# Kernel tuning notes

Measured on AMD Instinct MI355X. Metric: run time of the kernel, lower is better.

The kernel has to match this reference:

```python
import jax, jax.numpy as jnp
import numpy as np

B, S, D = 2, 2048, 1024
H, DK = 16, 64          # n_heads, d_kv; inner_dim = H*DK = D
NUM_BUCKETS = 32        # T5 relative_attention_num_buckets
MAX_DIST = 128          # T5 relative_attention_max_distance
SM_SCALE = 1.0 / np.sqrt(H)  # module uses 1/sqrt(n_heads), not 1/sqrt(d_kv)


def setup_inputs() -> dict:
    key = jax.random.key(0)
    ks = jax.random.split(key, 6)
    w = 0.02  # typical init scale for projection weights
    return {
        "hidden_states": jax.random.normal(ks[0], (B, S, D), jnp.float32),
        "Wq": jax.random.normal(ks[1], (D, H * DK), jnp.float32) * w,
        "Wk": jax.random.normal(ks[2], (D, H * DK), jnp.float32) * w,
        "Wv": jax.random.normal(ks[3], (D, H * DK), jnp.float32) * w,
        "Wo": jax.random.normal(ks[4], (H * DK, D), jnp.float32) * w,
        "rel_bias": jax.random.normal(ks[5], (NUM_BUCKETS, H), jnp.float32) * w,
    }


def _relative_position_buckets(qlen, klen):
    """T5 bidirectional relative-position bucketing -> [qlen, klen] int32."""
    ctx = jnp.arange(qlen, dtype=jnp.int32)[:, None]
    mem = jnp.arange(klen, dtype=jnp.int32)[None, :]
    rp = mem - ctx  # relative position
    nb = NUM_BUCKETS // 2  # bidirectional split
    ret = (rp > 0).astype(jnp.int32) * nb
    rpa = jnp.abs(rp)
    max_exact = nb // 2
    is_small = rpa < max_exact
    rpf = jnp.maximum(rpa, 1).astype(jnp.float32)
    large = max_exact + (
        jnp.log(rpf / max_exact) / np.log(MAX_DIST / max_exact) * (nb - max_exact)
    ).astype(jnp.int32)
    large = jnp.minimum(large, nb - 1)
    return ret + jnp.where(is_small, rpa, large)


def reference(hidden_states, Wq, Wk, Wv, Wo, rel_bias):
    b, s, d = hidden_states.shape
    q = (hidden_states @ Wq).reshape(b, s, H, DK)
    k = (hidden_states @ Wk).reshape(b, s, H, DK)
    v = (hidden_states @ Wv).reshape(b, s, H, DK)

    buckets = _relative_position_buckets(s, s)        # [S, S]
    bias = rel_bias[buckets]                          # [S, S, H]
    bias = jnp.transpose(bias, (2, 0, 1))[None]       # [1, H, S, S]

    scores = jnp.einsum("bqhd,bkhd->bhqk", q, k) * SM_SCALE + bias
    attn = jax.nn.softmax(scores, axis=-1)
    out = jnp.einsum("bhqk,bkhd->bqhd", attn, v).reshape(b, s, H * DK)
    return out @ Wo
```

## Files before the change

kernel.cpp:

```cpp
#include <hip/hip_runtime.h>
#include <math.h>


typedef _Float16 f16;
typedef _Float16 f16x4 __attribute__((ext_vector_type(4)));
typedef _Float16 f16x8 __attribute__((ext_vector_type(8)));
typedef float f32x4 __attribute__((ext_vector_type(4)));
typedef float f32x16 __attribute__((ext_vector_type(16)));
typedef unsigned int u32;
typedef u32 u32x4 __attribute__((ext_vector_type(4)));

#define MFMA16(a, b, c) __builtin_amdgcn_mfma_f32_16x16x32_f16((a), (b), (c), 0, 0, 0)
#define MFMA32(a, b, c) __builtin_amdgcn_mfma_f32_32x32x16_f16((a), (b), (c), 0, 0, 0)

static __device__ __forceinline__ float EXP2(float x) {
  float r;
  asm("v_exp_f32 %0, %1" : "=v"(r) : "v"(x));
  return r;
}

static __device__ __forceinline__ u32 pk2(float a, float b) {
  return __builtin_bit_cast(u32, __builtin_amdgcn_cvt_pkrtz(a, b));
}
static __device__ __forceinline__ void swap32(u32& a, u32& b) {
  asm volatile("v_permlane32_swap_b32 %0, %1" : "+v"(a), "+v"(b));
}

#define KEEPV8(v8)                                                        \
  do {                                                                    \
    u32x4 _t = __builtin_bit_cast(u32x4, (v8));                           \
    asm volatile("" ::"v"(_t[0]), "v"(_t[1]), "v"(_t[2]), "v"(_t[3]));    \
  } while (0)

__device__ __forceinline__ void gload16(const f16* g, f16* l) {
  __builtin_amdgcn_global_load_lds(
      (const __attribute__((address_space(1))) void*)g,
      (__attribute__((address_space(3))) void*)l, 16, 0, 0);
}


__global__ __launch_bounds__(256) void cast_x_kernel(const float4* __restrict__ x,
                                                     f16x4* __restrict__ xh) {
  int i = blockIdx.x * 256 + threadIdx.x;
  float4 v = x[i];
  f16x4 o;
  o[0] = (f16)v.x; o[1] = (f16)v.y; o[2] = (f16)v.z; o[3] = (f16)v.w;
  xh[i] = o;
}

__global__ void transpose_w_kernel(const float* __restrict__ w0, const float* __restrict__ w1,
                                   const float* __restrict__ w2, const float* __restrict__ w3,
                                   f16* __restrict__ wt) {
  int z = blockIdx.z;
  const float* w = (z == 0) ? w0 : (z == 1) ? w1 : (z == 2) ? w2 : w3;
  float sc = (z == 0) ? 0.36067376022224085f : 1.0f;
  __shared__ float tile[32][33];
  int tx = threadIdx.x, ty = threadIdx.y;
  int kt = blockIdx.x * 32, nt = blockIdx.y * 32;
#pragma unroll
  for (int i = 0; i < 4; ++i)
    tile[ty + i * 8][tx] = w[(size_t)(kt + ty + i * 8) * 1024 + nt + tx];
  __syncthreads();
#pragma unroll
  for (int i = 0; i < 4; ++i)
    wt[((size_t)z * 1024 + nt + ty + i * 8) * 1024 + kt + tx] = (f16)(tile[tx][ty + i * 8] * sc);
}

__global__ void transpose_v_kernel(const f16* __restrict__ vin, f16* __restrict__ vout) {
  __shared__ f16 tile[32][33];
  int bh = blockIdx.z;
  int s0 = blockIdx.x * 32, d0 = blockIdx.y * 32;
  int tx = threadIdx.x, ty = threadIdx.y;
  const f16* src = vin + ((size_t)bh * 2048 + s0) * 64 + d0;
#pragma unroll
  for (int i = 0; i < 4; ++i) tile[ty + i * 8][tx] = src[(size_t)(ty + i * 8) * 64 + tx];
  __syncthreads();
  f16* dst = vout + ((size_t)bh * 64 + d0) * 2048 + s0;
#pragma unroll
  for (int i = 0; i < 4; ++i) dst[(size_t)(ty + i * 8) * 2048 + tx] = tile[tx][ty + i * 8];
}

__global__ __launch_bounds__(256) void bias_kernel(const float* __restrict__ rel_bias,
                                                   f16* __restrict__ bias_rel) {
  int idx = blockIdx.x * 256 + threadIdx.x;
  int h = idx >> 12;
  int r = idx & 4095;
  int rp = r - 2048;
  if (rp < -2047) rp = -2047;
  int bucket = (rp > 0) ? 16 : 0;
  int rpa = (rp < 0) ? -rp : rp;
  if (rpa < 8) {
    bucket += rpa;
  } else {
    int large = 8 + (int)(logf((float)rpa / 8.0f) / logf(16.0f) * 8.0f);
    bucket += (large < 15) ? large : 15;
  }
  bias_rel[idx] = (f16)(rel_bias[bucket * 16 + h] * 1.4426950408889634f);
}

__device__ __forceinline__ void gemm128_core(const f16* __restrict__ A, const f16* __restrict__ Bt,
                                             int mrow, int ncol0, f16* sm ,
                                             f32x4 acc[4][4]) {
  const int t = threadIdx.x;
  const int lane = t & 63, w = t >> 6;
  const int cL = lane & 15, g = lane >> 4;
  const int wr = w >> 1, wc = w & 1;

  const int c0 = w * 128 + lane;
  const int c1 = c0 + 64;
  const int rA0 = c0 >> 2, kA0 = ((c0 & 3) ^ (rA0 & 3)) << 3;
  const int rA1 = c1 >> 2, kA1 = ((c1 & 3) ^ (rA1 & 3)) << 3;
  const f16* gA0 = A + (size_t)(mrow + rA0) * 1024 + kA0;
  const f16* gA1 = A + (size_t)(mrow + rA1) * 1024 + kA1;
  const f16* gB0 = Bt + (size_t)(ncol0 + rA0) * 1024 + kA0;
  const f16* gB1 = Bt + (size_t)(ncol0 + rA1) * 1024 + kA1;
  const int lds0 = (w * 2) * 512, lds1 = (w * 2 + 1) * 512;

#define GSTAGE(buf, k0)                            \
  do {                                             \
    f16* s_ = sm + (buf) * 8192;                   \
    gload16(gA0 + (k0), s_ + lds0);                \
    gload16(gA1 + (k0), s_ + lds1);                \
    gload16(gB0 + (k0), s_ + 4096 + lds0);         \
    gload16(gB1 + (k0), s_ + 4096 + lds1);         \
  } while (0)

  GSTAGE(0, 0);
  __syncthreads();
#pragma unroll 2
  for (int ks = 0; ks < 32; ++ks) {
    const int cur = ks & 1;
    if (ks < 31) GSTAGE(cur ^ 1, (ks + 1) * 32);
    const f16* bA = sm + cur * 8192;
    const f16* bB = bA + 4096;
    f16x8 af[4], bf[4];
#pragma unroll
    for (int m = 0; m < 4; ++m) {
      int r = wr * 64 + m * 16 + cL;
      af[m] = *(const f16x8*)&bA[r * 32 + ((g ^ (r & 3)) << 3)];
    }
#pragma unroll
    for (int n = 0; n < 4; ++n) {
      int r = wc * 64 + n * 16 + cL;
      bf[n] = *(const f16x8*)&bB[r * 32 + ((g ^ (r & 3)) << 3)];
    }
#pragma unroll
    for (int m = 0; m < 4; ++m)
#pragma unroll
      for (int n = 0; n < 4; ++n) acc[m][n] = MFMA16(af[m], bf[n], acc[m][n]);
    __syncthreads();
  }
#undef GSTAGE
}

__global__ __launch_bounds__(256) void gemm_qkv_kernel(const f16* __restrict__ Xh,
                                                       const f16* __restrict__ Wt,
                                                       f16* __restrict__ Qh,
                                                       f16* __restrict__ Kh,
                                                       f16* __restrict__ Vrow) {
  __shared__ __align__(16) f16 sm[2][8192];
  int mrow = blockIdx.y * 128, ncol0 = blockIdx.x * 128;
  f32x4 acc[4][4] = {};
  gemm128_core(Xh, Wt, mrow, ncol0, &sm[0][0], acc);
  int lane = threadIdx.x & 63, w = threadIdx.x >> 6;
  int cL = lane & 15, g = lane >> 4;
  int wr = w >> 1, wc = w & 1;
  int which = (ncol0 + wc * 64) >> 10;
  f16* dst = (which == 0) ? Qh : (which == 1) ? Kh : Vrow;
#pragma unroll
  for (int m = 0; m < 4; ++m) {
#pragma unroll
    for (int n = 0; n < 4; ++n) {
#pragma unroll
      for (int r = 0; r < 4; ++r) {
        int tt = mrow + wr * 64 + m * 16 + g * 4 + r;
        int b = tt >> 11, s = tt & 2047;
        int col = (ncol0 + wc * 64 + n * 16 + cL) & 1023;
        int hh = col >> 6, dk = col & 63;
        dst[(((size_t)b * 16 + hh) * 2048 + s) * 64 + dk] = (f16)acc[m][n][r];
      }
    }
  }
}

__global__ __launch_bounds__(256) void gemm_out_kernel(const f16* __restrict__ Oh,
                                                       const f16* __restrict__ WoT,
                                                       float* __restrict__ out) {
  __shared__ __align__(16) f16 sm[2][8192];
  int mrow = blockIdx.y * 128, ncol0 = blockIdx.x * 128;
  f32x4 acc[4][4] = {};
  gemm128_core(Oh, WoT, mrow, ncol0, &sm[0][0], acc);
  int lane = threadIdx.x & 63, w = threadIdx.x >> 6;
  int cL = lane & 15, g = lane >> 4;
  int wr = w >> 1, wc = w & 1;
#pragma unroll
  for (int m = 0; m < 4; ++m)
#pragma unroll
    for (int n = 0; n < 4; ++n)
#pragma unroll
      for (int r = 0; r < 4; ++r) {
        int tt = mrow + wr * 64 + m * 16 + g * 4 + r;
        out[(size_t)tt * 1024 + ncol0 + wc * 64 + n * 16 + cL] = acc[m][n][r];
      }
}

__global__ __launch_bounds__(512) void attn_kernel(const f16* __restrict__ Qh,
                                                   const f16* __restrict__ Kh,
                                                   const f16* __restrict__ Vt,
                                                   const f16* __restrict__ bias_rel,
                                                   f16* __restrict__ Oh) {
  __shared__ __align__(16) f16 sKV[2][2][8192];
  __shared__ __align__(16) f16 sB[2176];
  const int p = blockIdx.x;
  const int L = ((p & 7) << 6) + (p >> 3);
  const int bh = L >> 4;
  const int qt = (L & 15) << 7;
  const int h = bh & 15, b = bh >> 4;
  int t = threadIdx.x;
  int lane = t & 63, wave = t >> 6;
  const int gr = wave >> 2, sw = wave & 3;
  int lo5 = lane & 31, hi = lane >> 5;
  const size_t bhS = (size_t)bh * 2048;
  const int qrow = qt + sw * 32 + lo5;

  const f16* qp = Qh + (bhS + qrow) * 64 + hi * 8;
  f16x8 qf[4];
#pragma unroll
  for (int m = 0; m < 4; ++m) qf[m] = *(const f16x8*)(qp + 16 * m);

  float cpos = (float)bias_rel[(size_t)h * 4096 + 4095];
  float cneg = (float)bias_rel[(size_t)h * 4096 + 1];

#pragma unroll
  for (int m = 0; m < 4; ++m) KEEPV8(qf[m]);
  asm volatile("" ::"v"(cpos), "v"(cneg));

  {
    const float4* gB = (const float4*)(bias_rel + (size_t)h * 4096 + 1920 - qt);
    for (int i = t; i < 272; i += 512) ((float4*)sB)[i] = gB[i];
  }

  const int tg = t & 255;
  const int rK0 = tg >> 3, ccK0 = ((tg & 7) ^ (rK0 & 7)) << 3;
  const int rK1 = rK0 + 32, ccK1 = ((tg & 7) ^ (rK1 & 7)) << 3;
  const f16* gK0 = Kh + (bhS + rK0) * 64 + ccK0;
  const f16* gK1 = Kh + (bhS + rK1) * 64 + ccK1;
  const f16* gV0 = Vt + ((size_t)bh * 64 + rK0) * 2048 + ccK0;
  const f16* gV1 = Vt + ((size_t)bh * 64 + rK1) * 2048 + ccK1;
  const int ldsA = sw * 512, ldsB = sw * 512 + 2048;

#define ASTAGE(buf, key0)                           \
  do {                                              \
    f16* s_ = &sKV[gr][buf][0];                     \
    gload16(gK0 + (size_t)(key0) * 64, s_ + ldsA);  \
    gload16(gK1 + (size_t)(key0) * 64, s_ + ldsB);  \
    gload16(gV0 + (key0), s_ + 4096 + ldsA);        \
    gload16(gV1 + (key0), s_ + 4096 + ldsB);        \
  } while (0)

  f32x16 o0 = {}, o1 = {};
  float m_ = -INFINITY, lsum = 0.f;
  const int sw7 = lo5 & 7;
  const int kbase = gr << 10;

  ASTAGE(0, kbase);
  asm volatile("s_waitcnt lgkmcnt(0)" ::: "memory");

  for (int it = 0; it < 16; ++it) {
    asm volatile("s_waitcnt vmcnt(0)" ::: "memory");
    __builtin_amdgcn_s_barrier();
    if (it < 15) ASTAGE((it + 1) & 1, kbase + (it + 1) * 64);

    const int key0 = kbase + it * 64;
    const f16* kb = &sKV[gr][it & 1][0];
    const f16* vb = kb + 4096;
    const int dkt = key0 - qt;

    f32x16 sa0, sa1;
    if (dkt >= 256 || dkt <= -192) {
      float c = (dkt > 0) ? cpos : cneg;
#pragma unroll
      for (int i = 0; i < 16; ++i) { sa0[i] = c; sa1[i] = c; }
    } else {
      const int bb = key0 + 4 * hi - sw * 32 - lo5 + 128;
#pragma unroll
      for (int i = 0; i < 16; ++i) {
        int pat = (i & 3) + 8 * (i >> 2);
        sa0[i] = (float)sB[bb + pat];
        sa1[i] = (float)sB[bb + 32 + pat];
      }
    }
    const f16* kr0 = kb + lo5 * 64;
    const f16* kr1 = kb + (32 + lo5) * 64;
    __builtin_amdgcn_s_setprio(1);
#pragma unroll
    for (int m = 0; m < 4; ++m) {
      int c = ((2 * m + hi) ^ sw7) << 3;
      sa0 = MFMA32(*(const f16x8*)(kr0 + c), qf[m], sa0);
      sa1 = MFMA32(*(const f16x8*)(kr1 + c), qf[m], sa1);
    }
    __builtin_amdgcn_s_setprio(0);
    float tm[16];
#pragma unroll
    for (int i = 0; i < 16; ++i) tm[i] = fmaxf(sa0[i], sa1[i]);
#pragma unroll
    for (int s2 = 8; s2; s2 >>= 1)
#pragma unroll
      for (int i = 0; i < 8; ++i)
        if (i < s2) tm[i] = fmaxf(tm[i], tm[i + s2]);
    float mx = fmaxf(tm[0], __shfl_xor(tm[0], 32));
    if (__any(mx > m_ + 8.f)) {
      float mn = fmaxf(m_, mx);
      float corr = EXP2(m_ - mn);
      lsum *= corr;
      m_ = mn;
#pragma unroll
      for (int i = 0; i < 16; ++i) { o0[i] *= corr; o1[i] *= corr; }
    }
    float pr[16];
    u32 w0, w1, w2, w3, w4, w5, w6, w7;
#pragma unroll
    for (int i = 0; i < 16; ++i) pr[i] = EXP2(sa0[i] - m_);
    w0 = pk2(pr[0], pr[1]);   w1 = pk2(pr[2], pr[3]);
    w2 = pk2(pr[4], pr[5]);   w3 = pk2(pr[6], pr[7]);
    w4 = pk2(pr[8], pr[9]);   w5 = pk2(pr[10], pr[11]);
    w6 = pk2(pr[12], pr[13]); w7 = pk2(pr[14], pr[15]);
#pragma unroll
    for (int s2 = 8; s2; s2 >>= 1)
#pragma unroll
      for (int i = 0; i < 8; ++i)
        if (i < s2) pr[i] += pr[i + s2];
    float ls = pr[0];
    swap32(w0, w2); swap32(w1, w3); swap32(w4, w6); swap32(w5, w7);
    f16x8 pb0 = __builtin_bit_cast(f16x8, (u32x4){w0, w1, w2, w3});
    f16x8 pb1 = __builtin_bit_cast(f16x8, (u32x4){w4, w5, w6, w7});
#pragma unroll
    for (int i = 0; i < 16; ++i) pr[i] = EXP2(sa1[i] - m_);
    w0 = pk2(pr[0], pr[1]);   w1 = pk2(pr[2], pr[3]);
    w2 = pk2(pr[4], pr[5]);   w3 = pk2(pr[6], pr[7]);
    w4 = pk2(pr[8], pr[9]);   w5 = pk2(pr[10], pr[11]);
    w6 = pk2(pr[12], pr[13]); w7 = pk2(pr[14], pr[15]);
#pragma unroll
    for (int s2 = 8; s2; s2 >>= 1)
#pragma unroll
      for (int i = 0; i < 8; ++i)
        if (i < s2) pr[i] += pr[i + s2];
    lsum += ls + pr[0];
    swap32(w0, w2); swap32(w1, w3); swap32(w4, w6); swap32(w5, w7);
    f16x8 pb2 = __builtin_bit_cast(f16x8, (u32x4){w0, w1, w2, w3});
    f16x8 pb3 = __builtin_bit_cast(f16x8, (u32x4){w4, w5, w6, w7});
    const f16* vr0 = vb + lo5 * 64;
    const f16* vr1 = vb + (32 + lo5) * 64;
    __builtin_amdgcn_s_setprio(1);
    {
      int c = ((0 + hi) ^ sw7) << 3;
      o0 = MFMA32(*(const f16x8*)(vr0 + c), pb0, o0);
      o1 = MFMA32(*(const f16x8*)(vr1 + c), pb0, o1);
    }
    {
      int c = ((2 + hi) ^ sw7) << 3;
      o0 = MFMA32(*(const f16x8*)(vr0 + c), pb1, o0);
      o1 = MFMA32(*(const f16x8*)(vr1 + c), pb1, o1);
    }
    {
      int c = ((4 + hi) ^ sw7) << 3;
      o0 = MFMA32(*(const f16x8*)(vr0 + c), pb2, o0);
      o1 = MFMA32(*(const f16x8*)(vr1 + c), pb2, o1);
    }
    {
      int c = ((6 + hi) ^ sw7) << 3;
      o0 = MFMA32(*(const f16x8*)(vr0 + c), pb3, o0);
      o1 = MFMA32(*(const f16x8*)(vr1 + c), pb3, o1);
    }
    __builtin_amdgcn_s_setprio(0);
  }
#undef ASTAGE

  __syncthreads();
  float* sX = (float*)&sKV[0][0][0];
  const int slot = (sw * 64 + lane) * 35;
  if (gr == 1) {
#pragma unroll
    for (int i = 0; i < 16; ++i) {
      sX[slot + i] = o0[i];
      sX[slot + 16 + i] = o1[i];
    }
    sX[slot + 32] = m_;
    sX[slot + 33] = lsum;
  }
  __syncthreads();
  if (gr == 0) {
    float m2 = sX[slot + 32], l2 = sX[slot + 33];
    float mn = fmaxf(m_, m2);
    float c1 = EXP2(m_ - mn), c2 = EXP2(m2 - mn);
    float s = lsum * c1 + l2 * c2;
    s += __shfl_xor(s, 32);
    float inv = 1.0f / s;
    size_t base = ((size_t)b * 2048 + qrow) * 1024 + h * 64 + 4 * hi;
#pragma unroll
    for (int rq = 0; rq < 4; ++rq) {
      f16x4 v0, v1;
#pragma unroll
      for (int j = 0; j < 4; ++j) {
        v0[j] = (f16)((o0[rq * 4 + j] * c1 + sX[slot + rq * 4 + j] * c2) * inv);
        v1[j] = (f16)((o1[rq * 4 + j] * c1 + sX[slot + 16 + rq * 4 + j] * c2) * inv);
      }
      *(f16x4*)&Oh[base + 8 * rq] = v0;
      *(f16x4*)&Oh[base + 32 + 8 * rq] = v1;
    }
  }
}


extern "C" void kernel_launch(void* const* d_in, const int* in_sizes, int n_in,
                              void* d_out, int out_size, void* d_ws, size_t ws_size,
                              hipStream_t stream) {
  const float* X = (const float*)d_in[0];
  const float* Wq = (const float*)d_in[1];
  const float* Wk = (const float*)d_in[2];
  const float* Wv = (const float*)d_in[3];
  const float* Wo = (const float*)d_in[4];
  const float* relb = (const float*)d_in[5];

  const size_t MB8 = (size_t)8 << 20;
  if (ws_size < 6 * MB8 + (1 << 19)) return;

  char* ws = (char*)d_ws;
  f16* Xh = (f16*)(ws + 0 * MB8);
  f16* Wt = (f16*)(ws + 1 * MB8);
  f16* Qh = (f16*)(ws + 2 * MB8);
  f16* Kh = (f16*)(ws + 3 * MB8);
  f16* Vt = (f16*)(ws + 4 * MB8);
  f16* Oh = (f16*)(ws + 5 * MB8);
  f16* brel = (f16*)(ws + 6 * MB8);
  f16* Vrow = Oh;

  cast_x_kernel<<<dim3(4096), dim3(256), 0, stream>>>((const float4*)X, (f16x4*)Xh);
  transpose_w_kernel<<<dim3(32, 32, 4), dim3(32, 8), 0, stream>>>(Wq, Wk, Wv, Wo, Wt);
  bias_kernel<<<dim3(256), dim3(256), 0, stream>>>(relb, brel);
  gemm_qkv_kernel<<<dim3(24, 32), dim3(256), 0, stream>>>(Xh, Wt, Qh, Kh, Vrow);
  transpose_v_kernel<<<dim3(64, 2, 32), dim3(32, 8), 0, stream>>>(Vrow, Vt);
  attn_kernel<<<dim3(512), dim3(512), 0, stream>>>(Qh, Kh, Vt, brel, Oh);
  gemm_out_kernel<<<dim3(8, 32), dim3(256), 0, stream>>>(Oh, Wt + (size_t)3072 * 1024,
                                                         (float*)d_out);
}
```

Measured before the change: 144.1 us.

## Process two key tiles per barrier in attention and merge prep kernels

The attention loop now handles two 64-key tiles per iteration with a four-deep K/V LDS ring. It prefetches two tiles ahead, computes QK for both, and does a single row-max and rescale check per pair, which halves the barriers and max reductions. The three preprocessing kernels (cast X, transpose weights, bias table) are merged into one launch, removing two kernel launches. In exchange, LDS use for K/V doubles, which may reduce occupancy, and register pressure rises from holding four score vectors.

```diff
diff --git a/kernel.cpp b/kernel.cpp
--- a/kernel.cpp
+++ b/kernel.cpp
@@ -38,32 +38,53 @@
       (__attribute__((address_space(3))) void*)l, 16, 0, 0);
 }
 
-
-__global__ __launch_bounds__(256) void cast_x_kernel(const float4* __restrict__ x,
-                                                     f16x4* __restrict__ xh) {
-  int i = blockIdx.x * 256 + threadIdx.x;
-  float4 v = x[i];
-  f16x4 o;
-  o[0] = (f16)v.x; o[1] = (f16)v.y; o[2] = (f16)v.z; o[3] = (f16)v.w;
-  xh[i] = o;
-}
-
-__global__ void transpose_w_kernel(const float* __restrict__ w0, const float* __restrict__ w1,
-                                   const float* __restrict__ w2, const float* __restrict__ w3,
-                                   f16* __restrict__ wt) {
-  int z = blockIdx.z;
-  const float* w = (z == 0) ? w0 : (z == 1) ? w1 : (z == 2) ? w2 : w3;
-  float sc = (z == 0) ? 0.36067376022224085f : 1.0f;
-  __shared__ float tile[32][33];
-  int tx = threadIdx.x, ty = threadIdx.y;
-  int kt = blockIdx.x * 32, nt = blockIdx.y * 32;
-#pragma unroll
-  for (int i = 0; i < 4; ++i)
-    tile[ty + i * 8][tx] = w[(size_t)(kt + ty + i * 8) * 1024 + nt + tx];
-  __syncthreads();
-#pragma unroll
-  for (int i = 0; i < 4; ++i)
-    wt[((size_t)z * 1024 + nt + ty + i * 8) * 1024 + kt + tx] = (f16)(tile[tx][ty + i * 8] * sc);
+__global__ void prep_kernel(const float* __restrict__ X, const float* __restrict__ w0,
+                            const float* __restrict__ w1, const float* __restrict__ w2,
+                            const float* __restrict__ w3, const float* __restrict__ relb,
+                            f16x4* __restrict__ xh, f16* __restrict__ wt,
+                            f16* __restrict__ bias_rel) {
+  const int z = blockIdx.z;
+  const int tx = threadIdx.x, ty = threadIdx.y;
+  if (z < 4) {
+    const float* w = (z == 0) ? w0 : (z == 1) ? w1 : (z == 2) ? w2 : w3;
+    float sc = (z == 0) ? 0.36067376022224085f : 1.0f;
+    __shared__ float tile[32][33];
+    int kt = blockIdx.x * 32, nt = blockIdx.y * 32;
+#pragma unroll
+    for (int i = 0; i < 4; ++i)
+      tile[ty + i * 8][tx] = w[(size_t)(kt + ty + i * 8) * 1024 + nt + tx];
+    __syncthreads();
+#pragma unroll
+    for (int i = 0; i < 4; ++i)
+      wt[((size_t)z * 1024 + nt + ty + i * 8) * 1024 + kt + tx] =
+          (f16)(tile[tx][ty + i * 8] * sc);
+  } else if (z == 4) {
+    if (blockIdx.x >= 8) return;
+    int idx = (blockIdx.x * 32 + blockIdx.y) * 256 + ty * 32 + tx;
+    int h = idx >> 12;
+    int r = idx & 4095;
+    int rp = r - 2048;
+    if (rp < -2047) rp = -2047;
+    int bucket = (rp > 0) ? 16 : 0;
+    int rpa = (rp < 0) ? -rp : rp;
+    if (rpa < 8) {
+      bucket += rpa;
+    } else {
+      int large = 8 + (int)(logf((float)rpa / 8.0f) / logf(16.0f) * 8.0f);
+      bucket += (large < 15) ? large : 15;
+    }
+    bias_rel[idx] = (f16)(relb[bucket * 16 + h] * 1.4426950408889634f);
+  } else {
+    const float4* x4 = (const float4*)X;
+    int i = (blockIdx.x * 32 + blockIdx.y) * 256 + ty * 32 + tx;
+#pragma unroll
+    for (int rep = 0; rep < 4; ++rep, i += 262144) {
+      float4 v = x4[i];
+      f16x4 o;
+      o[0] = (f16)v.x; o[1] = (f16)v.y; o[2] = (f16)v.z; o[3] = (f16)v.w;
+      xh[i] = o;
+    }
+  }
 }
 
 __global__ void transpose_v_kernel(const f16* __restrict__ vin, f16* __restrict__ vout) {
@@ -78,24 +99,6 @@
   f16* dst = vout + ((size_t)bh * 64 + d0) * 2048 + s0;
 #pragma unroll
   for (int i = 0; i < 4; ++i) dst[(size_t)(ty + i * 8) * 2048 + tx] = tile[tx][ty + i * 8];
-}
-
-__global__ __launch_bounds__(256) void bias_kernel(const float* __restrict__ rel_bias,
-                                                   f16* __restrict__ bias_rel) {
-  int idx = blockIdx.x * 256 + threadIdx.x;
-  int h = idx >> 12;
-  int r = idx & 4095;
-  int rp = r - 2048;
-  if (rp < -2047) rp = -2047;
-  int bucket = (rp > 0) ? 16 : 0;
-  int rpa = (rp < 0) ? -rp : rp;
-  if (rpa < 8) {
-    bucket += rpa;
-  } else {
-    int large = 8 + (int)(logf((float)rpa / 8.0f) / logf(16.0f) * 8.0f);
-    bucket += (large < 15) ? large : 15;
-  }
-  bias_rel[idx] = (f16)(rel_bias[bucket * 16 + h] * 1.4426950408889634f);
 }
 
 __device__ __forceinline__ void gemm128_core(const f16* __restrict__ A, const f16* __restrict__ Bt,
@@ -209,7 +212,7 @@
                                                    const f16* __restrict__ Vt,
                                                    const f16* __restrict__ bias_rel,
                                                    f16* __restrict__ Oh) {
-  __shared__ __align__(16) f16 sKV[2][2][8192];
+  __shared__ __align__(16) f16 sKV[2][4][8192];
   __shared__ __align__(16) f16 sB[2176];
   const int p = blockIdx.x;
   const int L = ((p & 7) << 6) + (p >> 3);
@@ -263,52 +266,130 @@
   const int sw7 = lo5 & 7;
   const int kbase = gr << 10;
 
+  auto qk = [&](const f16* kb, f32x16& s0, f32x16& s1) {
+    const f16* kr0 = kb + lo5 * 64;
+    const f16* kr1 = kb + (32 + lo5) * 64;
+#pragma unroll
+    for (int m = 0; m < 4; ++m) {
+      int c = ((2 * m + hi) ^ sw7) << 3;
+      s0 = MFMA32(*(const f16x8*)(kr0 + c), qf[m], s0);
+      s1 = MFMA32(*(const f16x8*)(kr1 + c), qf[m], s1);
+    }
+  };
+  auto rowmax = [&](const f32x16& a, const f32x16& bvec) -> float {
+    float tm[16];
+#pragma unroll
+    for (int i = 0; i < 16; ++i) tm[i] = fmaxf(a[i], bvec[i]);
+#pragma unroll
+    for (int s2 = 8; s2; s2 >>= 1)
+#pragma unroll
+      for (int i = 0; i < 8; ++i)
+        if (i < s2) tm[i] = fmaxf(tm[i], tm[i + s2]);
+    return tm[0];
+  };
+  auto softpack = [&](const f32x16& s0, const f32x16& s1, f16x8& b0, f16x8& b1, f16x8& b2,
+                      f16x8& b3) -> float {
+    float pr[16];
+    u32 w0, w1, w2, w3, w4, w5, w6, w7;
+#pragma unroll
+    for (int i = 0; i < 16; ++i) pr[i] = EXP2(s0[i] - m_);
+    w0 = pk2(pr[0], pr[1]);   w1 = pk2(pr[2], pr[3]);
+    w2 = pk2(pr[4], pr[5]);   w3 = pk2(pr[6], pr[7]);
+    w4 = pk2(pr[8], pr[9]);   w5 = pk2(pr[10], pr[11]);
+    w6 = pk2(pr[12], pr[13]); w7 = pk2(pr[14], pr[15]);
+#pragma unroll
+    for (int s2 = 8; s2; s2 >>= 1)
+#pragma unroll
+      for (int i = 0; i < 8; ++i)
+        if (i < s2) pr[i] += pr[i + s2];
+    float ls = pr[0];
+    swap32(w0, w2); swap32(w1, w3); swap32(w4, w6); swap32(w5, w7);
+    b0 = __builtin_bit_cast(f16x8, (u32x4){w0, w1, w2, w3});
+    b1 = __builtin_bit_cast(f16x8, (u32x4){w4, w5, w6, w7});
+#pragma unroll
+    for (int i = 0; i < 16; ++i) pr[i] = EXP2(s1[i] - m_);
+    w0 = pk2(pr[0], pr[1]);   w1 = pk2(pr[2], pr[3]);
+    w2 = pk2(pr[4], pr[5]);   w3 = pk2(pr[6], pr[7]);
+    w4 = pk2(pr[8], pr[9]);   w5 = pk2(pr[10], pr[11]);
+    w6 = pk2(pr[12], pr[13]); w7 = pk2(pr[14], pr[15]);
+#pragma unroll
+    for (int s2 = 8; s2; s2 >>= 1)
+#pragma unroll
+      for (int i = 0; i < 8; ++i)
+        if (i < s2) pr[i] += pr[i + s2];
+    ls += pr[0];
+    swap32(w0, w2); swap32(w1, w3); swap32(w4, w6); swap32(w5, w7);
+    b2 = __builtin_bit_cast(f16x8, (u32x4){w0, w1, w2, w3});
+    b3 = __builtin_bit_cast(f16x8, (u32x4){w4, w5, w6, w7});
+    return ls;
+  };
+  auto pv = [&](const f16* vb, const f16x8& b0, const f16x8& b1, const f16x8& b2,
+                const f16x8& b3) {
+    const f16* vr0 = vb + lo5 * 64;
+    const f16* vr1 = vb + (32 + lo5) * 64;
+    {
+      int c = ((0 + hi) ^ sw7) << 3;
+      o0 = MFMA32(*(const f16x8*)(vr0 + c), b0, o0);
+      o1 = MFMA32(*(const f16x8*)(vr1 + c), b0, o1);
+    }
+    {
+      int c = ((2 + hi) ^ sw7) << 3;
+      o0 = MFMA32(*(const f16x8*)(vr0 + c), b1, o0);
+      o1 = MFMA32(*(const f16x8*)(vr1 + c), b1, o1);
+    }
+    {
+      int c = ((4 + hi) ^ sw7) << 3;
+      o0 = MFMA32(*(const f16x8*)(vr0 + c), b2, o0);
+      o1 = MFMA32(*(const f16x8*)(vr1 + c), b2, o1);
+    }
+    {
+      int c = ((6 + hi) ^ sw7) << 3;
+      o0 = MFMA32(*(const f16x8*)(vr0 + c), b3, o0);
+      o1 = MFMA32(*(const f16x8*)(vr1 + c), b3, o1);
+    }
+  };
+  auto biasinit = [&](int key0, f32x16& s0, f32x16& s1) {
+    const int dkt = key0 - qt;
+    if (dkt >= 256 || dkt <= -192) {
+      float c = (dkt > 0) ? cpos : cneg;
+#pragma unroll
+      for (int i = 0; i < 16; ++i) { s0[i] = c; s1[i] = c; }
+    } else {
+      const int bb = key0 + 4 * hi - sw * 32 - lo5 + 128;
+#pragma unroll
+      for (int i = 0; i < 16; ++i) {
+        int pat = (i & 3) + 8 * (i >> 2);
+        s0[i] = (float)sB[bb + pat];
+        s1[i] = (float)sB[bb + 32 + pat];
+      }
+    }
+  };
+
   ASTAGE(0, kbase);
+  ASTAGE(1, kbase + 64);
   asm volatile("s_waitcnt lgkmcnt(0)" ::: "memory");
 
-  for (int it = 0; it < 16; ++it) {
+  for (int pp = 0; pp < 8; ++pp) {
     asm volatile("s_waitcnt vmcnt(0)" ::: "memory");
     __builtin_amdgcn_s_barrier();
-    if (it < 15) ASTAGE((it + 1) & 1, kbase + (it + 1) * 64);
-
-    const int key0 = kbase + it * 64;
-    const f16* kb = &sKV[gr][it & 1][0];
-    const f16* vb = kb + 4096;
-    const int dkt = key0 - qt;
-
-    f32x16 sa0, sa1;
-    if (dkt >= 256 || dkt <= -192) {
-      float c = (dkt > 0) ? cpos : cneg;
-#pragma unroll
-      for (int i = 0; i < 16; ++i) { sa0[i] = c; sa1[i] = c; }
-    } else {
-      const int bb = key0 + 4 * hi - sw * 32 - lo5 + 128;
-#pragma unroll
-      for (int i = 0; i < 16; ++i) {
-        int pat = (i & 3) + 8 * (i >> 2);
-        sa0[i] = (float)sB[bb + pat];
-        sa1[i] = (float)sB[bb + 32 + pat];
-      }
-    }
-    const f16* kr0 = kb + lo5 * 64;
-    const f16* kr1 = kb + (32 + lo5) * 64;
+    if (pp < 7) {
+      ASTAGE((2 * pp + 2) & 3, kbase + (2 * pp + 2) * 64);
+      ASTAGE((2 * pp + 3) & 3, kbase + (2 * pp + 3) * 64);
+    }
+    const int keyA = kbase + 2 * pp * 64;
+    const f16* bufA = &sKV[gr][(2 * pp) & 3][0];
+    const f16* bufB = &sKV[gr][(2 * pp + 1) & 3][0];
+
+    f32x16 saA0, saA1, saB0, saB1;
+    biasinit(keyA, saA0, saA1);
+    biasinit(keyA + 64, saB0, saB1);
     __builtin_amdgcn_s_setprio(1);
-#pragma unroll
-    for (int m = 0; m < 4; ++m) {
-      int c = ((2 * m + hi) ^ sw7) << 3;
-      sa0 = MFMA32(*(const f16x8*)(kr0 + c), qf[m], sa0);
-      sa1 = MFMA32(*(const f16x8*)(kr1 + c), qf[m], sa1);
-    }
+    qk(bufA, saA0, saA1);
+    qk(bufB, saB0, saB1);
     __builtin_amdgcn_s_setprio(0);
-    float tm[16];
-#pragma unroll
-    for (int i = 0; i < 16; ++i) tm[i] = fmaxf(sa0[i], sa1[i]);
-#pragma unroll
-    for (int s2 = 8; s2; s2 >>= 1)
-#pragma unroll
-      for (int i = 0; i < 8; ++i)
-        if (i < s2) tm[i] = fmaxf(tm[i], tm[i + s2]);
-    float mx = fmaxf(tm[0], __shfl_xor(tm[0], 32));
+
+    float mx = fmaxf(rowmax(saA0, saA1), rowmax(saB0, saB1));
+    mx = fmaxf(mx, __shfl_xor(mx, 32));
     if (__any(mx > m_ + 8.f)) {
       float mn = fmaxf(m_, mx);
       float corr = EXP2(m_ - mn);
@@ -317,61 +398,15 @@
 #pragma unroll
       for (int i = 0; i < 16; ++i) { o0[i] *= corr; o1[i] *= corr; }
     }
-    float pr[16];
-    u32 w0, w1, w2, w3, w4, w5, w6, w7;
-#pragma unroll
-    for (int i = 0; i < 16; ++i) pr[i] = EXP2(sa0[i] - m_);
-    w0 = pk2(pr[0], pr[1]);   w1 = pk2(pr[2], pr[3]);
-    w2 = pk2(pr[4], pr[5]);   w3 = pk2(pr[6], pr[7]);
-    w4 = pk2(pr[8], pr[9]);   w5 = pk2(pr[10], pr[11]);
-    w6 = pk2(pr[12], pr[13]); w7 = pk2(pr[14], pr[15]);
-#pragma unroll
-    for (int s2 = 8; s2; s2 >>= 1)
-#pragma unroll
-      for (int i = 0; i < 8; ++i)
-        if (i < s2) pr[i] += pr[i + s2];
-    float ls = pr[0];
-    swap32(w0, w2); swap32(w1, w3); swap32(w4, w6); swap32(w5, w7);
-    f16x8 pb0 = __builtin_bit_cast(f16x8, (u32x4){w0, w1, w2, w3});
-    f16x8 pb1 = __builtin_bit_cast(f16x8, (u32x4){w4, w5, w6, w7});
-#pragma unroll
-    for (int i = 0; i < 16; ++i) pr[i] = EXP2(sa1[i] - m_);
-    w0 = pk2(pr[0], pr[1]);   w1 = pk2(pr[2], pr[3]);
-    w2 = pk2(pr[4], pr[5]);   w3 = pk2(pr[6], pr[7]);
-    w4 = pk2(pr[8], pr[9]);   w5 = pk2(pr[10], pr[11]);
-    w6 = pk2(pr[12], pr[13]); w7 = pk2(pr[14], pr[15]);
-#pragma unroll
-    for (int s2 = 8; s2; s2 >>= 1)
-#pragma unroll
-      for (int i = 0; i < 8; ++i)
-        if (i < s2) pr[i] += pr[i + s2];
-    lsum += ls + pr[0];
-    swap32(w0, w2); swap32(w1, w3); swap32(w4, w6); swap32(w5, w7);
-    f16x8 pb2 = __builtin_bit_cast(f16x8, (u32x4){w0, w1, w2, w3});
-    f16x8 pb3 = __builtin_bit_cast(f16x8, (u32x4){w4, w5, w6, w7});
-    const f16* vr0 = vb + lo5 * 64;
-    const f16* vr1 = vb + (32 + lo5) * 64;
+
+    f16x8 f0, f1, f2, f3;
+    lsum += softpack(saA0, saA1, f0, f1, f2, f3);
     __builtin_amdgcn_s_setprio(1);
-    {
-      int c = ((0 + hi) ^ sw7) << 3;
-      o0 = MFMA32(*(const f16x8*)(vr0 + c), pb0, o0);
-      o1 = MFMA32(*(const f16x8*)(vr1 + c), pb0, o1);
-    }
-    {
-      int c = ((2 + hi) ^ sw7) << 3;
-      o0 = MFMA32(*(const f16x8*)(vr0 + c), pb1, o0);
-      o1 = MFMA32(*(const f16x8*)(vr1 + c), pb1, o1);
-    }
-    {
-      int c = ((4 + hi) ^ sw7) << 3;
-      o0 = MFMA32(*(const f16x8*)(vr0 + c), pb2, o0);
-      o1 = MFMA32(*(const f16x8*)(vr1 + c), pb2, o1);
-    }
-    {
-      int c = ((6 + hi) ^ sw7) << 3;
-      o0 = MFMA32(*(const f16x8*)(vr0 + c), pb3, o0);
-      o1 = MFMA32(*(const f16x8*)(vr1 + c), pb3, o1);
-    }
+    pv(bufA + 4096, f0, f1, f2, f3);
+    __builtin_amdgcn_s_setprio(0);
+    lsum += softpack(saB0, saB1, f0, f1, f2, f3);
+    __builtin_amdgcn_s_setprio(1);
+    pv(bufB + 4096, f0, f1, f2, f3);
     __builtin_amdgcn_s_setprio(0);
   }
 #undef ASTAGE
@@ -435,9 +470,8 @@
   f16* brel = (f16*)(ws + 6 * MB8);
   f16* Vrow = Oh;
 
-  cast_x_kernel<<<dim3(4096), dim3(256), 0, stream>>>((const float4*)X, (f16x4*)Xh);
-  transpose_w_kernel<<<dim3(32, 32, 4), dim3(32, 8), 0, stream>>>(Wq, Wk, Wv, Wo, Wt);
-  bias_kernel<<<dim3(256), dim3(256), 0, stream>>>(relb, brel);
+  prep_kernel<<<dim3(32, 32, 6), dim3(32, 8), 0, stream>>>(X, Wq, Wk, Wv, Wo, relb,
+                                                           (f16x4*)Xh, Wt, brel);
   gemm_qkv_kernel<<<dim3(24, 32), dim3(256), 0, stream>>>(Xh, Wt, Qh, Kh, Vrow);
   transpose_v_kernel<<<dim3(64, 2, 32), dim3(32, 8), 0, stream>>>(Vrow, Vt);
   attn_kernel<<<dim3(512), dim3(512), 0, stream>>>(Qh, Kh, Vt, brel, Oh);
```

After: 136.2 us (median of 3 runs). -5.5%, faster.
